# Optimization experiments

Measured on AMD Instinct MI355X. Metric: run time of the kernel, lower is better.

## Reference

```python
import jax, jax.numpy as jnp
import numpy as np

N_NODES = 50000


def setup_inputs() -> dict:
    key = jax.random.key(0)
    ks = jax.random.split(key, 6)
    E = 640000
    H = 128
    data = jax.random.normal(ks[0], (N_NODES, H), dtype=jnp.float32)
    edge = jax.random.randint(ks[1], (2, E), 0, N_NODES, dtype=jnp.int64)
    att = jax.random.uniform(ks[2], (E,), dtype=jnp.float32)
    w1 = jax.random.normal(ks[3], (2 * H, H), dtype=jnp.float32) * (1.0 / np.sqrt(2 * H))
    b1 = jnp.zeros((H,), dtype=jnp.float32)
    w2 = jax.random.normal(ks[4], (2 * H, H), dtype=jnp.float32) * (1.0 / np.sqrt(2 * H))
    b2 = jnp.zeros((H,), dtype=jnp.float32)
    return {"data": data, "edge": edge, "att": att, "w1": w1, "b1": b1, "w2": w2, "b2": b2}


def _simple_conv_mean_cat(x, edge, att):
    # PyG SimpleConv(aggr='mean', combine_root='cat') with scalar edge weights.
    src, dst = edge[0], edge[1]
    msgs = x[src] * att[:, None]                               # [E, H] gather + scale
    summed = jax.ops.segment_sum(msgs, dst, num_segments=N_NODES)   # [N, H]
    deg = jax.ops.segment_sum(jnp.ones_like(att), dst, num_segments=N_NODES)  # [N]
    agg = summed / jnp.maximum(deg, 1.0)[:, None]              # mean over incoming edges
    return jnp.concatenate([x, agg], axis=-1)                  # [N, 2H]


def reference(data, edge, att, w1, b1, w2, b2):
    out = _simple_conv_mean_cat(data, edge, att)
    out = jax.nn.relu(out @ w1 + b1)
    out = _simple_conv_mean_cat(out, edge, att)
    out = jax.nn.relu(out @ w2 + b2)
    return out
```

## Files before the change

kernel.cpp:

```cpp
#include <hip/hip_runtime.h>


#define HDIM 128
#define CAP 32
#define FCH 2048

typedef __bf16 bf16x8 __attribute__((ext_vector_type(8)));
typedef float floatx4 __attribute__((ext_vector_type(4)));

__device__ __forceinline__ unsigned short f2bf(float f) {
    unsigned int u = __float_as_uint(f);
    unsigned int r = (u + 0x7fff + ((u >> 16) & 1)) >> 16;
    return (unsigned short)r;
}
__device__ __forceinline__ float bf2f(unsigned short b) {
    return __uint_as_float((unsigned int)b << 16);
}

__global__ __launch_bounds__(256) void k_fill(const int* __restrict__ edge, int E,
                                              const float* __restrict__ att,
                                              int* __restrict__ cursor,
                                              int* __restrict__ ovf_cnt,
                                              unsigned int* __restrict__ pse,
                                              float4* __restrict__ ovf, int rsize,
                                              int nfb,
                                              const float* __restrict__ data,
                                              unsigned short* __restrict__ data_bf, int n4,
                                              int cb, int NN,
                                              const float* __restrict__ w1,
                                              unsigned short* __restrict__ w1t,
                                              const float* __restrict__ w2,
                                              unsigned short* __restrict__ w2t) {
    int b = blockIdx.x;
    int t = threadIdx.x;
    if (b < nfb) {
        __shared__ int s_or;
        if (t == 0) s_or = 0;
        __syncthreads();
        int nw = 2 * E < 512 ? 2 * E : 512;
        int iw = t * 2 + 1;
        int vw = (iw < nw) ? edge[iw] : 0;
        if (vw != 0) atomicOr(&s_or, 1);
        __syncthreads();
        int sh = (s_or == 0) ? 1 : 0;

        int r = b & 7;
        int c = b >> 3;
        int lo = r * rsize;
        int hi = lo + rsize;
        int e0 = c * FCH;
        int e1 = min(E, e0 + FCH);
        for (int e = e0 + t; e < e1; e += 256) {
            int d = edge[(size_t)(E + e) << sh];
            if (d >= lo && d < hi) {
                int s = edge[(size_t)e << sh];
                float a = att[e];
                int slot = atomicAdd(&cursor[d], 1);
                if (slot < CAP) {
                    unsigned int rec = ((unsigned int)f2bf(a) << 16) | (unsigned int)(s & 0xffff);
                    pse[(size_t)d * CAP + slot] = rec;
                } else {
                    int oi = atomicAdd(ovf_cnt, 1);
                    ovf[oi] = make_float4(__int_as_float(d), __int_as_float(s), a, 0.f);
                }
            }
        }
        return;
    }
    b -= nfb;
    if (b < cb) {
        int i = b * 256 + t;
        if (i < n4) {
            float4 v = ((const float4*)data)[i];
            ushort4 o;
            o.x = f2bf(v.x); o.y = f2bf(v.y); o.z = f2bf(v.z); o.w = f2bf(v.w);
            int nn = i >> 5;
            int c4 = i & 31;
            *(ushort4*)(data_bf + (((size_t)(c4 >> 3) * NN + nn) << 5) + ((c4 & 7) << 2)) = o;
        }
        return;
    }
    b -= cb;
    {
        const float* w = (b < 128) ? w1 : w2;
        unsigned short* wt = (b < 128) ? w1t : w2t;
        int bb = (b < 128) ? b : b - 128;
        int idx = bb * 256 + t;
        int k = idx >> 7;
        int n = idx & 127;
        wt[(size_t)n * 256 + k] = f2bf(w[(size_t)k * 128 + n]);
    }
}

__global__ __launch_bounds__(256) void k_agg(const unsigned short* __restrict__ x,
                                             const unsigned int* __restrict__ pse,
                                             const int* __restrict__ cursor,
                                             const int* __restrict__ ovf_cnt,
                                             const float4* __restrict__ ovf,
                                             unsigned short* __restrict__ agg, int N) {
    __shared__ __align__(16) unsigned int s_rec[64 * 36];
    int tid = threadIdx.x;
    int pass = blockIdx.y;
    int base = blockIdx.x * 64;

#pragma unroll
    for (int k = 0; k < 2; ++k) {
        int idx4 = tid + k * 256;
        int i = idx4 >> 3;
        int j0 = (idx4 & 7) << 2;
        int nn = base + i;
        uint4 v = make_uint4(0u, 0u, 0u, 0u);
        if (nn < N) v = *(const uint4*)(pse + ((size_t)nn << 5) + j0);
        *(uint4*)(&s_rec[i * 36 + j0]) = v;
    }
    __syncthreads();

    int lane = tid & 63;
    int wave = tid >> 6;
    int q = lane >> 2;
    int l4 = lane & 3;
    int ni = wave * 16 + q;
    int n = base + ni;
    bool valid = n < N;
    int deg = valid ? cursor[n] : 0;
    int m = min(deg, CAP);

    const unsigned short* xs = x + (((size_t)pass * N) << 5) + (l4 << 3);
    const unsigned int* rp = &s_rec[ni * 36];
    float s0 = 0.f, s1 = 0.f, s2 = 0.f, s3 = 0.f, s4 = 0.f, s5 = 0.f, s6 = 0.f, s7 = 0.f;

#define ACC8(u, a)                                                  \
    do {                                                            \
        s0 = fmaf(bf2f((unsigned short)((u).x & 0xffff)), (a), s0); \
        s1 = fmaf(bf2f((unsigned short)((u).x >> 16)), (a), s1);    \
        s2 = fmaf(bf2f((unsigned short)((u).y & 0xffff)), (a), s2); \
        s3 = fmaf(bf2f((unsigned short)((u).y >> 16)), (a), s3);    \
        s4 = fmaf(bf2f((unsigned short)((u).z & 0xffff)), (a), s4); \
        s5 = fmaf(bf2f((unsigned short)((u).z >> 16)), (a), s5);    \
        s6 = fmaf(bf2f((unsigned short)((u).w & 0xffff)), (a), s6); \
        s7 = fmaf(bf2f((unsigned short)((u).w >> 16)), (a), s7);    \
    } while (0)

    for (int j = 0; j < m; j += 2) {
        unsigned int r0 = rp[j];
        unsigned int r1 = rp[j + 1];
        r1 = (j + 1 < m) ? r1 : 0u;
        uint4 u0 = *(const uint4*)(xs + ((size_t)(r0 & 0xffffu) << 5));
        uint4 u1 = *(const uint4*)(xs + ((size_t)(r1 & 0xffffu) << 5));
        float a0 = __uint_as_float(r0 & 0xffff0000u);
        float a1 = __uint_as_float(r1 & 0xffff0000u);
        ACC8(u0, a0);
        ACC8(u1, a1);
    }

    int oc = ovf_cnt[0];
    if (oc > 0 && valid) {
        for (int k = 0; k < oc; ++k) {
            float4 f = ovf[k];
            if (__float_as_int(f.x) == n) {
                uint4 u = *(const uint4*)(xs + ((size_t)__float_as_int(f.y) << 5));
                ACC8(u, f.z);
            }
        }
    }
#undef ACC8

    if (valid) {
        float inv = 1.0f / fmaxf((float)deg, 1.0f);
        uint4 o;
        o.x = (unsigned int)f2bf(s0 * inv) | ((unsigned int)f2bf(s1 * inv) << 16);
        o.y = (unsigned int)f2bf(s2 * inv) | ((unsigned int)f2bf(s3 * inv) << 16);
        o.z = (unsigned int)f2bf(s4 * inv) | ((unsigned int)f2bf(s5 * inv) << 16);
        o.w = (unsigned int)f2bf(s6 * inv) | ((unsigned int)f2bf(s7 * inv) << 16);
        *(uint4*)(agg + ((((size_t)pass * N) + n) << 5) + (l4 << 3)) = o;
    }
}

__global__ __launch_bounds__(256) void k_gemm_mfma(const unsigned short* __restrict__ X,
                                                   const unsigned short* __restrict__ AGG,
                                                   const unsigned short* __restrict__ Wt,
                                                   const float* __restrict__ bias,
                                                   float* __restrict__ outF,
                                                   unsigned short* __restrict__ outB,
                                                   int M) {
    __shared__ __align__(16) unsigned short sW[128 * 256];

    int tid = threadIdx.x;
    int wave = tid >> 6;
    int lane = tid & 63;
    int l16 = lane & 15;
    int quad = lane >> 4;

#pragma unroll
    for (int it = 0; it < 16; ++it) {
        int chunk = it * 256 + tid;
        int row = chunk >> 5;
        int c5 = chunk & 31;
        int kc = c5 >> 2;
        int q = c5 & 3;
        int qs = q ^ (row & 3);
        uint4 v = *(const uint4*)(Wt + (size_t)chunk * 8);
        *(uint4*)(sW + row * 256 + kc * 32 + qs * 8) = v;
    }

    int row = blockIdx.x * 64 + wave * 16 + l16;
    int rowA = min(row, M - 1);
    const unsigned short* xb0 = X + ((size_t)rowA << 5) + quad * 8;
    const unsigned short* ab0 = AGG + ((size_t)rowA << 5) + quad * 8;
    bf16x8 af[8];
#pragma unroll
    for (int kc = 0; kc < 4; ++kc) af[kc] = *(const bf16x8*)(xb0 + ((size_t)kc * M << 5));
#pragma unroll
    for (int kc = 0; kc < 4; ++kc) af[kc + 4] = *(const bf16x8*)(ab0 + ((size_t)kc * M << 5));

    __syncthreads();

    floatx4 acc[8];
#pragma unroll
    for (int c = 0; c < 8; ++c) acc[c] = (floatx4){0.f, 0.f, 0.f, 0.f};

#pragma unroll
    for (int kc = 0; kc < 8; ++kc) {
#pragma unroll
        for (int c = 0; c < 8; ++c) {
            int rb = c * 16 + l16;
            int qs = quad ^ (rb & 3);
            bf16x8 bfr = *(const bf16x8*)(sW + rb * 256 + kc * 32 + qs * 8);
            acc[c] = __builtin_amdgcn_mfma_f32_16x16x32_bf16(af[kc], bfr, acc[c], 0, 0, 0);
        }
    }

    int orow0 = blockIdx.x * 64 + wave * 16 + quad * 4;
#pragma unroll
    for (int c = 0; c < 8; ++c) {
        int col = c * 16 + l16;
        float bv = bias[col];
#pragma unroll
        for (int r = 0; r < 4; ++r) {
            int orow = orow0 + r;
            if (orow < M) {
                float v = fmaxf(acc[c][r] + bv, 0.f);
                if (outF) outF[(size_t)orow * 128 + col] = v;
                else outB[(((size_t)(col >> 5) * M + orow) << 5) + (col & 31)] = f2bf(v);
            }
        }
    }
}

extern "C" void kernel_launch(void* const* d_in, const int* in_sizes, int n_in,
                              void* d_out, int out_size, void* d_ws, size_t ws_size,
                              hipStream_t stream) {
    const float* data = (const float*)d_in[0];
    const int* edge = (const int*)d_in[1];
    const float* att = (const float*)d_in[2];
    const float* w1 = (const float*)d_in[3];
    const float* b1 = (const float*)d_in[4];
    const float* w2 = (const float*)d_in[5];
    const float* b2 = (const float*)d_in[6];

    const int N = in_sizes[0] / HDIM;
    const int E = in_sizes[1] / 2;

    char* ws = (char*)d_ws;
    size_t o = 0;
    auto carve = [&](size_t bytes) -> char* {
        char* r = ws + o;
        o = (o + bytes + 255) & ~(size_t)255;
        return r;
    };
    int* cursor = (int*)carve((size_t)(N + 4) * 4);
    int* ovf_cnt = cursor + N;
    unsigned int* pse = (unsigned int*)carve((size_t)N * CAP * 4);
    float4* ovf = (float4*)carve((size_t)E * 16);
    unsigned short* data_bf = (unsigned short*)carve((size_t)N * 128 * 2);
    unsigned short* w1t = (unsigned short*)carve(256 * 128 * 2);
    unsigned short* w2t = (unsigned short*)carve(256 * 128 * 2);
    unsigned short* agg_bf = (unsigned short*)carve((size_t)N * 128 * 2);
    unsigned short* out1_bf = (unsigned short*)carve((size_t)N * 128 * 2);
    float* outF = (float*)d_out;

    hipMemsetAsync(cursor, 0, (size_t)(N + 4) * 4, stream);

    int rsize = (N + 7) / 8;
    int nch = (E + FCH - 1) / FCH;
    int nfb = nch * 8;
    int n4 = N * 128 / 4;
    int cb = (n4 + 255) / 256;
    k_fill<<<nfb + cb + 256, 256, 0, stream>>>(edge, E, att, cursor, ovf_cnt, pse, ovf,
                                               rsize, nfb, data, data_bf, n4, cb, N,
                                               w1, w1t, w2, w2t);

    dim3 gag((N + 63) / 64, 4);
    int gb = (N + 63) / 64;
    k_agg<<<gag, 256, 0, stream>>>(data_bf, pse, cursor, ovf_cnt, ovf, agg_bf, N);
    k_gemm_mfma<<<gb, 256, 0, stream>>>(data_bf, agg_bf, w1t, b1, nullptr, out1_bf, N);
    k_agg<<<gag, 256, 0, stream>>>(out1_bf, pse, cursor, ovf_cnt, ovf, agg_bf, N);
    k_gemm_mfma<<<gb, 256, 0, stream>>>(out1_bf, agg_bf, w2t, b2, outF, nullptr, N);
}
```

Baseline: 221.4 us.

## Simplify edge bucketing to one pass and deepen gather unroll in aggregation

The fill phase drops the 8-way destination-range partitioning, in which every block re-read its edge chunk and kept only edges for one node range. Each block now handles 512 edges in a single pass with two edges per thread, so edge indices are read once instead of eight times. In exchange, atomics on destination cursors are spread across all nodes rather than localized, so the pse writes lose locality. The aggregation loop now issues 8 independent row gathers per iteration instead of 2, raising memory-level parallelism at the cost of more registers. The extra record reads past m still stay inside the 36-entry padded shared buffer.

```diff
diff --git a/kernel.cpp b/kernel.cpp
--- a/kernel.cpp
+++ b/kernel.cpp
@@ -3,7 +3,6 @@
 
 #define HDIM 128
 #define CAP 32
-#define FCH 2048
 
 typedef __bf16 bf16x8 __attribute__((ext_vector_type(8)));
 typedef float floatx4 __attribute__((ext_vector_type(4)));
@@ -22,7 +21,7 @@
                                               int* __restrict__ cursor,
                                               int* __restrict__ ovf_cnt,
                                               unsigned int* __restrict__ pse,
-                                              float4* __restrict__ ovf, int rsize,
+                                              float4* __restrict__ ovf,
                                               int nfb,
                                               const float* __restrict__ data,
                                               unsigned short* __restrict__ data_bf, int n4,
@@ -44,25 +43,33 @@
         __syncthreads();
         int sh = (s_or == 0) ? 1 : 0;
 
-        int r = b & 7;
-        int c = b >> 3;
-        int lo = r * rsize;
-        int hi = lo + rsize;
-        int e0 = c * FCH;
-        int e1 = min(E, e0 + FCH);
-        for (int e = e0 + t; e < e1; e += 256) {
-            int d = edge[(size_t)(E + e) << sh];
-            if (d >= lo && d < hi) {
-                int s = edge[(size_t)e << sh];
-                float a = att[e];
-                int slot = atomicAdd(&cursor[d], 1);
-                if (slot < CAP) {
-                    unsigned int rec = ((unsigned int)f2bf(a) << 16) | (unsigned int)(s & 0xffff);
-                    pse[(size_t)d * CAP + slot] = rec;
-                } else {
-                    int oi = atomicAdd(ovf_cnt, 1);
-                    ovf[oi] = make_float4(__int_as_float(d), __int_as_float(s), a, 0.f);
-                }
+        int e0 = b * 512;
+        int eA = e0 + t;
+        int eB = e0 + 256 + t;
+        int dA = (eA < E) ? edge[(size_t)(E + eA) << sh] : -1;
+        int dB = (eB < E) ? edge[(size_t)(E + eB) << sh] : -1;
+        int sA = (eA < E) ? edge[(size_t)eA << sh] : 0;
+        int sB = (eB < E) ? edge[(size_t)eB << sh] : 0;
+        float aA = (eA < E) ? att[eA] : 0.f;
+        float aB = (eB < E) ? att[eB] : 0.f;
+        if (dA >= 0) {
+            int slot = atomicAdd(&cursor[dA], 1);
+            if (slot < CAP) {
+                unsigned int rec = ((unsigned int)f2bf(aA) << 16) | (unsigned int)(sA & 0xffff);
+                pse[(size_t)dA * CAP + slot] = rec;
+            } else {
+                int oi = atomicAdd(ovf_cnt, 1);
+                ovf[oi] = make_float4(__int_as_float(dA), __int_as_float(sA), aA, 0.f);
+            }
+        }
+        if (dB >= 0) {
+            int slot = atomicAdd(&cursor[dB], 1);
+            if (slot < CAP) {
+                unsigned int rec = ((unsigned int)f2bf(aB) << 16) | (unsigned int)(sB & 0xffff);
+                pse[(size_t)dB * CAP + slot] = rec;
+            } else {
+                int oi = atomicAdd(ovf_cnt, 1);
+                ovf[oi] = make_float4(__int_as_float(dB), __int_as_float(sB), aB, 0.f);
             }
         }
         return;
@@ -141,16 +148,20 @@
         s7 = fmaf(bf2f((unsigned short)((u).w >> 16)), (a), s7);    \
     } while (0)
 
-    for (int j = 0; j < m; j += 2) {
-        unsigned int r0 = rp[j];
-        unsigned int r1 = rp[j + 1];
-        r1 = (j + 1 < m) ? r1 : 0u;
-        uint4 u0 = *(const uint4*)(xs + ((size_t)(r0 & 0xffffu) << 5));
-        uint4 u1 = *(const uint4*)(xs + ((size_t)(r1 & 0xffffu) << 5));
-        float a0 = __uint_as_float(r0 & 0xffff0000u);
-        float a1 = __uint_as_float(r1 & 0xffff0000u);
-        ACC8(u0, a0);
-        ACC8(u1, a1);
+    for (int j = 0; j < m; j += 8) {
+        unsigned int rr[8];
+#pragma unroll
+        for (int k = 0; k < 8; ++k) {
+            unsigned int r = rp[j + k];
+            rr[k] = (j + k < m) ? r : 0u;
+        }
+        uint4 uu[8];
+#pragma unroll
+        for (int k = 0; k < 8; ++k)
+            uu[k] = *(const uint4*)(xs + ((size_t)(rr[k] & 0xffffu) << 5));
+#pragma unroll
+        for (int k = 0; k < 8; ++k)
+            ACC8(uu[k], __uint_as_float(rr[k] & 0xffff0000u));
     }
 
     int oc = ovf_cnt[0];
@@ -281,13 +292,11 @@
 
     hipMemsetAsync(cursor, 0, (size_t)(N + 4) * 4, stream);
 
-    int rsize = (N + 7) / 8;
-    int nch = (E + FCH - 1) / FCH;
-    int nfb = nch * 8;
+    int nfb = (E + 511) / 512;
     int n4 = N * 128 / 4;
     int cb = (n4 + 255) / 256;
     k_fill<<<nfb + cb + 256, 256, 0, stream>>>(edge, E, att, cursor, ovf_cnt, pse, ovf,
-                                               rsize, nfb, data, data_bf, n4, cb, N,
+                                               nfb, data, data_bf, n4, cb, N,
                                                w1, w1t, w2, w2t);
 
     dim3 gag((N + 63) / 64, 4);
```

Result: faster. 215.5 us (-2.7%).
